# Kernel tuning notes

Hardware: AMD Instinct MI355X
Metric: run time of the kernel (lower is better)

## Reference

```python
import jax, jax.numpy as jnp
import numpy as np
from jax import lax

B, H, W = 8, 512, 512


def setup_inputs() -> dict:
    key = jax.random.key(0)
    k1, k2, k3, k4, k5 = jax.random.split(key, 5)
    img = jax.random.uniform(k1, (B, 3, H, W), jnp.float32)
    omega = 0.8 + 0.15 * jax.random.uniform(k2, (B, 1), jnp.float32)
    atmospheric_light = 0.5 + 0.5 * jax.random.uniform(k3, (B, 3), jnp.float32)
    L_low = 2.0 * jax.random.uniform(k4, (B, 1), jnp.float32)          # percent in [0,2)
    L_high = 95.0 + 4.0 * jax.random.uniform(k5, (B, 1), jnp.float32)  # percent in [95,99)
    guided_radius = 15  # python int, uniform across batch (original clamps to [1,50])
    return {"img": img, "omega": omega, "atmospheric_light": atmospheric_light,
            "L_low": L_low, "L_high": L_high, "guided_radius": guided_radius}


def _box_filter(x, r):
    # reflect-pad + mean over (2r+1)x(2r+1) window, separable (exactly avg_pool2d on reflect-padded input)
    k = 2 * r + 1
    xp = jnp.pad(x, ((0, 0), (0, 0), (r, r), (r, r)), mode='reflect')
    s = lax.reduce_window(xp, 0.0, lax.add, (1, 1, k, 1), (1, 1, 1, 1), 'VALID')
    s = lax.reduce_window(s, 0.0, lax.add, (1, 1, 1, k), (1, 1, 1, 1), 'VALID')
    return s / (k * k)


def _forward(img, omega, atmospheric_light, L_low, L_high, r):
    eps = 0.5
    Bb, Cc, Hh, Ww = img.shape
    A = atmospheric_light.reshape(Bb, 3, 1, 1)
    # initial transmission: t = 1 - omega * min_c(I/A)
    dark = jnp.min(img / (A + 1e-8), axis=1, keepdims=True)           # (B,1,H,W)
    t0 = 1.0 - omega.reshape(Bb, 1, 1, 1) * dark
    # gradient constraint (weights from t0, applied to shifted copies)
    wx = jnp.exp(-jnp.abs(t0[:, :, :, 1:] - t0[:, :, :, :-1]))
    tx = jnp.concatenate([t0[:, :, :, :1], t0[:, :, :, :-1] * wx], axis=3)
    wy = jnp.exp(-jnp.abs(t0[:, :, 1:, :] - t0[:, :, :-1, :]))
    tg = jnp.concatenate([tx[:, :, :1, :], tx[:, :, :-1, :] * wy], axis=2)
    # guided filter with grayscale guide
    rgb_w = jnp.array([0.299, 0.587, 0.114], dtype=img.dtype).reshape(1, 3, 1, 1)
    gray = jnp.sum(img * rgb_w, axis=1, keepdims=True)                # (B,1,H,W)
    mI = _box_filter(gray, r)
    mp = _box_filter(tg, r)
    mIp = _box_filter(gray * tg, r)
    cov_Ip = mIp - mI * mp
    var_I = _box_filter(gray * gray, r) - mI * mI
    a = cov_Ip / (var_I + eps)
    b = mp - a * mI
    t_final = jnp.clip(_box_filter(a, r) * gray + _box_filter(b, r), 0.1, 1.0)
    # restoration
    J = jnp.clip((img - A) / (t_final + 1e-8) + A, 0.0, 1.0)
    # percentile color stretch (vectorized over B and C)
    n = Hh * Ww
    svals = jnp.sort(J.reshape(Bb, Cc, n), axis=-1)
    li = jnp.clip((L_low / 100.0 * n).astype(jnp.int32), 0, n - 1)    # (B,1)
    hi = jnp.clip((L_high / 100.0 * n).astype(jnp.int32), 0, n - 1)
    p_low = jnp.take_along_axis(svals, jnp.broadcast_to(li[:, :, None], (Bb, Cc, 1)), axis=-1).reshape(Bb, Cc, 1, 1)
    p_high = jnp.take_along_axis(svals, jnp.broadcast_to(hi[:, :, None], (Bb, Cc, 1)), axis=-1).reshape(Bb, Cc, 1, 1)
    out = (jnp.clip(J, p_low, p_high) - p_low) / (p_high - p_low + 1e-8)
    return jnp.clip(out, 0.0, 1.0)


def reference(img, omega, atmospheric_light, L_low, L_high, guided_radius):
    r = max(1, min(int(guided_radius), 50))
    return _forward(img, omega, atmospheric_light, L_low, L_high, r)
```

## Files before the change

### kernel.cpp

```cpp
#include <hip/hip_runtime.h>
#include <cstdint>

constexpr int Bb = 8, Hh = 512, Ww = 512;
constexpr int HWn = Hh * Ww;
constexpr int CH1  = 8;
constexpr int CH23 = 16;
constexpr int CHK4 = 8;
constexpr int NBIN = 1024;

__device__ __forceinline__ int reflect_idx(int p, int n) {
    p = (p < 0) ? -p : p;
    return (p < n) ? p : (2 * n - 2 - p);
}
__device__ __forceinline__ int clamp_r(const int* rad) {
    int r = rad[0];
    return (r < 1) ? 1 : ((r > 50) ? 50 : r);
}

__global__ __launch_bounds__(512) void k1_stats_h(
    const float* __restrict__ img, const float* __restrict__ omega,
    const float* __restrict__ atm, const int* __restrict__ rad,
    float4* __restrict__ hq, unsigned int* __restrict__ histzero)
{
    const int tile = blockIdx.x;
    const int b = blockIdx.y;
    const int y0 = tile * CH1;
    const int j = threadIdx.x;
    const int fbid = b * gridDim.x + tile;
    if (fbid < 48) histzero[fbid * 512 + j] = 0u;
    const int r = clamp_r(rad);

    __shared__ float t0buf[2][512];
    __shared__ float4 Pb[512];
    __shared__ float4 wsum[8];

    const float om = omega[b];
    const float iA0 = 1.0f / (atm[b*3+0] + 1e-8f);
    const float iA1 = 1.0f / (atm[b*3+1] + 1e-8f);
    const float iA2 = 1.0f / (atm[b*3+2] + 1e-8f);
    const float* imb = img + (size_t)b * 3 * HWn;

    {
        const int yp = (y0 > 0) ? (y0 - 1) : 0;
        float r1 = imb[0*HWn + yp*Ww + j];
        float g1 = imb[1*HWn + yp*Ww + j];
        float b1 = imb[2*HWn + yp*Ww + j];
        t0buf[0][j] = 1.0f - om * fminf(fminf(r1*iA0, g1*iA1), b1*iA2);
    }
    __syncthreads();

    const int lane = j & 63, wv = j >> 6;
    int pv = 0;
    for (int k = 0; k < CH1; ++k) {
        const int y = y0 + k;
        float r0 = imb[0*HWn + y*Ww + j];
        float g0 = imb[1*HWn + y*Ww + j];
        float b0 = imb[2*HWn + y*Ww + j];
        float t0c = 1.0f - om * fminf(fminf(r0*iA0, g0*iA1), b0*iA2);
        float gr = 0.299f*r0 + 0.587f*g0 + 0.114f*b0;
        const float* t0p = t0buf[pv];
        t0buf[pv^1][j] = t0c;
        float tpj = t0p[j];
        float tx  = (j == 0) ? t0p[0] : t0p[j-1] * __expf(-fabsf(tpj - t0p[j-1]));
        float tgv = (y == 0) ? tx : tx * __expf(-fabsf(t0c - tpj));

        float4 incl;
        incl.x = gr; incl.y = tgv; incl.z = gr * tgv; incl.w = gr * gr;
        #pragma unroll
        for (int off = 1; off < 64; off <<= 1) {
            float ux = __shfl_up(incl.x, off);
            float uy = __shfl_up(incl.y, off);
            float uz = __shfl_up(incl.z, off);
            float uw = __shfl_up(incl.w, off);
            if (lane >= off) { incl.x += ux; incl.y += uy; incl.z += uz; incl.w += uw; }
        }
        if (lane == 63) wsum[wv] = incl;
        __syncthreads();
        float4 o4; o4.x = 0.f; o4.y = 0.f; o4.z = 0.f; o4.w = 0.f;
        #pragma unroll
        for (int w = 0; w < 7; ++w) {
            if (w < wv) {
                float4 t = wsum[w];
                o4.x += t.x; o4.y += t.y; o4.z += t.z; o4.w += t.w;
            }
        }
        float4 P; P.x = incl.x + o4.x; P.y = incl.y + o4.y; P.z = incl.z + o4.z; P.w = incl.w + o4.w;
        Pb[j] = P;
        __syncthreads();

        const int lo = j - r, hi = j + r;
        float4 s = Pb[(hi > 511) ? 511 : hi];
        if (lo > 0) {
            float4 t = Pb[lo-1];
            s.x -= t.x; s.y -= t.y; s.z -= t.z; s.w -= t.w;
        }
        if (lo < 0) {
            float4 t = Pb[r - j], u = Pb[0];
            s.x += t.x - u.x; s.y += t.y - u.y; s.z += t.z - u.z; s.w += t.w - u.w;
        }
        if (hi > 511) {
            float4 t = Pb[510], u = Pb[1021 - j - r];
            s.x += t.x - u.x; s.y += t.y - u.y; s.z += t.z - u.z; s.w += t.w - u.w;
        }
        hq[((size_t)b * Hh + y) * Ww + j] = s;
        pv ^= 1;
    }
}

__global__ __launch_bounds__(512) void k23_ab_h(
    const float4* __restrict__ hq, const int* __restrict__ rad,
    float2* __restrict__ hab)
{
    const int b  = blockIdx.y;
    const int y0 = blockIdx.x * CH23;
    const int j  = threadIdx.x;
    const int r  = clamp_r(rad);
    const float ikk = 1.0f / (float)((2*r+1) * (2*r+1));
    const int lane = j & 63, wv = j >> 6;

    __shared__ float2 Pb8[CH23][512];
    __shared__ float2 wsum8[CH23][8];

    const float4* hqb = hq + (size_t)b * Hh * Ww + j;
    float4 s; s.x = 0.f; s.y = 0.f; s.z = 0.f; s.w = 0.f;
    if (r == 15) {
        #pragma unroll
        for (int d = -15; d <= 15; ++d) {
            int m = reflect_idx(y0 + d, Hh);
            float4 v = hqb[(size_t)m * Ww];
            s.x += v.x; s.y += v.y; s.z += v.z; s.w += v.w;
        }
    } else {
        for (int d = -r; d <= r; ++d) {
            int m = reflect_idx(y0 + d, Hh);
            float4 v = hqb[(size_t)m * Ww];
            s.x += v.x; s.y += v.y; s.z += v.z; s.w += v.w;
        }
    }
    float av[CH23], bv[CH23];
    #pragma unroll
    for (int k = 0; k < CH23; ++k) {
        int y = y0 + k;
        float mI = s.x * ikk, mp = s.y * ikk, mIp = s.z * ikk, mII = s.w * ikk;
        float a = (mIp - mI * mp) / (mII - mI * mI + 0.5f);
        av[k] = a;
        bv[k] = mp - a * mI;
        int yin  = reflect_idx(y + 1 + r, Hh);
        int yout = reflect_idx(y - r, Hh);
        float4 vi = hqb[(size_t)yin  * Ww];
        float4 vo = hqb[(size_t)yout * Ww];
        s.x += vi.x - vo.x; s.y += vi.y - vo.y; s.z += vi.z - vo.z; s.w += vi.w - vo.w;
    }

    float ix[CH23], iy[CH23];
    #pragma unroll
    for (int k = 0; k < CH23; ++k) {
        float sx = av[k], sy = bv[k];
        #pragma unroll
        for (int off = 1; off < 64; off <<= 1) {
            float ux = __shfl_up(sx, off);
            float uy = __shfl_up(sy, off);
            if (lane >= off) { sx += ux; sy += uy; }
        }
        ix[k] = sx; iy[k] = sy;
        if (lane == 63) { wsum8[k][wv].x = sx; wsum8[k][wv].y = sy; }
    }
    __syncthreads();

    #pragma unroll
    for (int k = 0; k < CH23; ++k) {
        float ox = 0.f, oy = 0.f;
        #pragma unroll
        for (int w = 0; w < 7; ++w) {
            if (w < wv) { float2 t = wsum8[k][w]; ox += t.x; oy += t.y; }
        }
        Pb8[k][j].x = ix[k] + ox;
        Pb8[k][j].y = iy[k] + oy;
    }
    __syncthreads();

    const int lo = j - r, hi = j + r;
    const int him = (hi > 511) ? 511 : hi;
    #pragma unroll
    for (int k = 0; k < CH23; ++k) {
        float2 hs = Pb8[k][him];
        if (lo > 0)   { float2 t = Pb8[k][lo-1];  hs.x -= t.x; hs.y -= t.y; }
        if (lo < 0)   { float2 t = Pb8[k][r-j], u = Pb8[k][0];
                        hs.x += t.x - u.x; hs.y += t.y - u.y; }
        if (hi > 511) { float2 t = Pb8[k][510], u = Pb8[k][1021-j-r];
                        hs.x += t.x - u.x; hs.y += t.y - u.y; }
        hab[((size_t)b * Hh + (y0 + k)) * Ww + j] = hs;
    }
}

__global__ __launch_bounds__(256) void k4_final_v(
    const float4* __restrict__ hab4, const float2* __restrict__ img2,
    const float* __restrict__ atm, const int* __restrict__ rad,
    float2* __restrict__ J2, unsigned int* __restrict__ hist)
{
    const int b   = blockIdx.y;
    const int y0  = blockIdx.x * CHK4;
    const int tid = threadIdx.x;
    const int r   = clamp_r(rad);
    const float ikk = 1.0f / (float)((2*r+1) * (2*r+1));
    const int HP4 = Ww / 2;
    const int CP2 = HWn / 2;
    const int RP2 = Ww / 2;

    __shared__ unsigned int lh[3 * NBIN];
    for (int i = tid; i < 3 * NBIN; i += 256) lh[i] = 0u;
    __syncthreads();

    const float A0 = atm[b*3+0], A1 = atm[b*3+1], A2 = atm[b*3+2];
    const float2* imb = img2 + (size_t)b * 3 * CP2;
    float2*       Jb  = J2   + (size_t)b * 3 * CP2;
    const float4* habb = hab4 + (size_t)b * Hh * HP4 + tid;

    float2 V0, V1;
    V0.x = 0.f; V0.y = 0.f; V1.x = 0.f; V1.y = 0.f;
    if (r == 15) {
        #pragma unroll
        for (int d = -15; d <= 15; ++d) {
            int m = reflect_idx(y0 + d, Hh);
            float4 h = habb[(size_t)m * HP4];
            V0.x += h.x; V0.y += h.y; V1.x += h.z; V1.y += h.w;
        }
    } else {
        for (int d = -r; d <= r; ++d) {
            int m = reflect_idx(y0 + d, Hh);
            float4 h = habb[(size_t)m * HP4];
            V0.x += h.x; V0.y += h.y; V1.x += h.z; V1.y += h.w;
        }
    }

    unsigned int clo0 = 0, chi0 = 0, clo1 = 0, chi1 = 0, clo2 = 0, chi2 = 0;

    #pragma unroll
    for (int k = 0; k < CHK4; ++k) {
        const int y = y0 + k;
        const int yin  = reflect_idx(y + 1 + r, Hh);
        const int yout = reflect_idx(y - r, Hh);
        float4 hi4 = habb[(size_t)yin  * HP4];
        float4 ho4 = habb[(size_t)yout * HP4];
        const size_t po = (size_t)y * RP2 + tid;
        float2 c0 = imb[0*CP2 + po];
        float2 c1 = imb[1*CP2 + po];
        float2 c2 = imb[2*CP2 + po];

        float jr[2], jg[2], jb[2];
        {
            float g_ = 0.299f*c0.x + 0.587f*c1.x + 0.114f*c2.x;
            float t  = fminf(fmaxf((V0.x * g_ + V0.y) * ikk, 0.1f), 1.0f);
            float it = 1.0f / (t + 1e-8f);
            jr[0] = fminf(fmaxf((c0.x - A0) * it + A0, 0.f), 1.f);
            jg[0] = fminf(fmaxf((c1.x - A1) * it + A1, 0.f), 1.f);
            jb[0] = fminf(fmaxf((c2.x - A2) * it + A2, 0.f), 1.f);
        }
        {
            float g_ = 0.299f*c0.y + 0.587f*c1.y + 0.114f*c2.y;
            float t  = fminf(fmaxf((V1.x * g_ + V1.y) * ikk, 0.1f), 1.0f);
            float it = 1.0f / (t + 1e-8f);
            jr[1] = fminf(fmaxf((c0.y - A0) * it + A0, 0.f), 1.f);
            jg[1] = fminf(fmaxf((c1.y - A1) * it + A1, 0.f), 1.f);
            jb[1] = fminf(fmaxf((c2.y - A2) * it + A2, 0.f), 1.f);
        }
        Jb[0*CP2 + po] = make_float2(jr[0], jr[1]);
        Jb[1*CP2 + po] = make_float2(jg[0], jg[1]);
        Jb[2*CP2 + po] = make_float2(jb[0], jb[1]);

        #pragma unroll
        for (int q = 0; q < 2; ++q) {
            int bR = (int)(jr[q] * (float)NBIN); bR = (bR > NBIN-1) ? NBIN-1 : bR;
            if (bR == 0) clo0++; else if (bR == NBIN-1) chi0++; else atomicAdd(&lh[0*NBIN + bR], 1u);
            int bG = (int)(jg[q] * (float)NBIN); bG = (bG > NBIN-1) ? NBIN-1 : bG;
            if (bG == 0) clo1++; else if (bG == NBIN-1) chi1++; else atomicAdd(&lh[1*NBIN + bG], 1u);
            int bB = (int)(jb[q] * (float)NBIN); bB = (bB > NBIN-1) ? NBIN-1 : bB;
            if (bB == 0) clo2++; else if (bB == NBIN-1) chi2++; else atomicAdd(&lh[2*NBIN + bB], 1u);
        }

        V0.x += hi4.x - ho4.x; V0.y += hi4.y - ho4.y;
        V1.x += hi4.z - ho4.z; V1.y += hi4.w - ho4.w;
    }

    if (clo0) atomicAdd(&lh[0*NBIN],            clo0);
    if (chi0) atomicAdd(&lh[0*NBIN + NBIN - 1], chi0);
    if (clo1) atomicAdd(&lh[1*NBIN],            clo1);
    if (chi1) atomicAdd(&lh[1*NBIN + NBIN - 1], chi1);
    if (clo2) atomicAdd(&lh[2*NBIN],            clo2);
    if (chi2) atomicAdd(&lh[2*NBIN + NBIN - 1], chi2);
    __syncthreads();

    const size_t hb = (size_t)b * 3 * NBIN;
    for (int i = tid; i < 3 * NBIN; i += 256) {
        unsigned int v = lh[i];
        if (v) atomicAdd(&hist[hb + i], v);
    }
}

__global__ __launch_bounds__(256) void k6_norm(
    float4* __restrict__ J4, const unsigned int* __restrict__ hist,
    const float* __restrict__ L_low, const float* __restrict__ L_high)
{
    const int bc  = blockIdx.x >> 6;
    const int sub = blockIdx.x & 63;
    const int b   = bc / 3;
    __shared__ float sp[2];

    if (threadIdx.x < 64) {
        const int lane = threadIdx.x;
        const unsigned int* hb = hist + (size_t)bc * NBIN;
        unsigned int loc[NBIN / 64];
        unsigned int lsum = 0;
        #pragma unroll
        for (int i = 0; i < NBIN / 64; ++i) { loc[i] = hb[lane * (NBIN/64) + i]; lsum += loc[i]; }
        unsigned int incl = lsum;
        #pragma unroll
        for (int off = 1; off < 64; off <<= 1) {
            unsigned int v = __shfl_up(incl, off);
            if (lane >= off) incl += v;
        }
        unsigned int excl = incl - lsum;
        #pragma unroll
        for (int t = 0; t < 2; ++t) {
            float L = t ? L_high[b] : L_low[b];
            int k = (int)(L * (1.0f / 100.0f) * (float)HWn);
            k = (k < 0) ? 0 : ((k > HWn - 1) ? HWn - 1 : k);
            if ((unsigned int)k >= excl && (unsigned int)k < incl) {
                unsigned int c = excl;
                #pragma unroll
                for (int i = 0; i < NBIN / 64; ++i) {
                    if ((unsigned int)k < c + loc[i]) {
                        sp[t] = ((float)(lane * (NBIN/64) + i) + 0.5f) * (1.0f / (float)NBIN);
                        break;
                    }
                    c += loc[i];
                }
            }
        }
    }
    __syncthreads();

    const float l = sp[0], h = sp[1];
    const float inv = 1.0f / (h - l + 1e-8f);
    float4* base = J4 + (size_t)bc * (HWn / 4) + (size_t)sub * 1024;
    #pragma unroll
    for (int s = 0; s < 4; ++s) {
        const int idx = threadIdx.x + s * 256;
        float4 v = base[idx];
        v.x = fminf(fmaxf((fminf(fmaxf(v.x, l), h) - l) * inv, 0.f), 1.f);
        v.y = fminf(fmaxf((fminf(fmaxf(v.y, l), h) - l) * inv, 0.f), 1.f);
        v.z = fminf(fmaxf((fminf(fmaxf(v.z, l), h) - l) * inv, 0.f), 1.f);
        v.w = fminf(fmaxf((fminf(fmaxf(v.w, l), h) - l) * inv, 0.f), 1.f);
        base[idx] = v;
    }
}

extern "C" void kernel_launch(void* const* d_in, const int* in_sizes, int n_in,
                              void* d_out, int out_size, void* d_ws, size_t ws_size,
                              hipStream_t stream)
{
    const float* img    = (const float*)d_in[0];
    const float* omega  = (const float*)d_in[1];
    const float* atm    = (const float*)d_in[2];
    const float* L_low  = (const float*)d_in[3];
    const float* L_high = (const float*)d_in[4];
    const int*   rad    = (const int*)d_in[5];
    float* J  = (float*)d_out;
    float* ws = (float*)d_ws;

    const size_t F = (size_t)Bb * HWn;
    float4* hq  = (float4*)ws;
    float2* hab = (float2*)(ws + 4 * F);
    unsigned int* hist = (unsigned int*)(ws + 6 * F);

    k1_stats_h<<<dim3(Hh/CH1,  Bb), 512, 0, stream>>>(img, omega, atm, rad, hq, hist);
    k23_ab_h  <<<dim3(Hh/CH23, Bb), 512, 0, stream>>>(hq, rad, hab);
    k4_final_v<<<dim3(Hh/CHK4, Bb), 256, 0, stream>>>((const float4*)hab, (const float2*)img, atm, rad, (float2*)J, hist);
    k6_norm   <<<24 * 64, 256, 0, stream>>>((float4*)J, hist, L_low, L_high);
}
```

Baseline: 171.3 us.

## Replace vertical sliding-window sums with chunked prefix sums plus per-chunk totals

```diff
diff --git a/kernel.cpp b/kernel.cpp
--- a/kernel.cpp
+++ b/kernel.cpp
@@ -4,9 +4,10 @@
 constexpr int Bb = 8, Hh = 512, Ww = 512;
 constexpr int HWn = Hh * Ww;
 constexpr int CH1  = 8;
-constexpr int CH23 = 16;
-constexpr int CHK4 = 8;
+constexpr int CH23 = 8;
+constexpr int CHK4 = 4;
 constexpr int NBIN = 1024;
+constexpr int NCHK = Hh / 8;
 
 __device__ __forceinline__ int reflect_idx(int p, int n) {
     p = (p < 0) ? -p : p;
@@ -16,11 +17,47 @@
     int r = rad[0];
     return (r < 1) ? 1 : ((r > 50) ? 50 : r);
 }
+__device__ __forceinline__ float4 f4add(float4 a, float4 b) {
+    return make_float4(a.x + b.x, a.y + b.y, a.z + b.z, a.w + b.w);
+}
+__device__ __forceinline__ float4 f4sub(float4 a, float4 b) {
+    return make_float4(a.x - b.x, a.y - b.y, a.z - b.z, a.w - b.w);
+}
+
+__device__ __forceinline__ float4 ps_range(const float4* __restrict__ P,
+                                           const float4* __restrict__ T,
+                                           int a, int b, int pitch) {
+    float4 res = P[(size_t)b * pitch];
+    int cs;
+    if (a > 0) {
+        res = f4sub(res, P[(size_t)(a - 1) * pitch]);
+        cs = (a - 1) >> 3;
+    } else {
+        cs = 0;
+    }
+    const int cb = b >> 3;
+    for (int c = cs; c < cb; ++c)
+        res = f4add(res, T[(size_t)c * pitch]);
+    return res;
+}
+
+__device__ __forceinline__ float4 win_sum(const float4* __restrict__ P,
+                                          const float4* __restrict__ T,
+                                          int y, int r, int pitch) {
+    const int lo = y - r, hi = y + r;
+    const int a = lo < 0 ? 0 : lo;
+    const int b = hi > Hh - 1 ? Hh - 1 : hi;
+    float4 s = ps_range(P, T, a, b, pitch);
+    if (lo < 0)      s = f4add(s, ps_range(P, T, 1, -lo, pitch));
+    if (hi > Hh - 1) s = f4add(s, ps_range(P, T, 2 * Hh - 2 - hi, Hh - 2, pitch));
+    return s;
+}
 
 __global__ __launch_bounds__(512) void k1_stats_h(
     const float* __restrict__ img, const float* __restrict__ omega,
     const float* __restrict__ atm, const int* __restrict__ rad,
-    float4* __restrict__ hq, unsigned int* __restrict__ histzero)
+    float4* __restrict__ P1, float4* __restrict__ T1,
+    unsigned int* __restrict__ histzero)
 {
     const int tile = blockIdx.x;
     const int b = blockIdx.y;
@@ -51,6 +88,7 @@
 
     const int lane = j & 63, wv = j >> 6;
     int pv = 0;
+    float4 pacc = make_float4(0.f, 0.f, 0.f, 0.f);
     for (int k = 0; k < CH1; ++k) {
         const int y = y0 + k;
         float r0 = imb[0*HWn + y*Ww + j];
@@ -76,40 +114,32 @@
         }
         if (lane == 63) wsum[wv] = incl;
         __syncthreads();
-        float4 o4; o4.x = 0.f; o4.y = 0.f; o4.z = 0.f; o4.w = 0.f;
+        float4 o4 = make_float4(0.f, 0.f, 0.f, 0.f);
         #pragma unroll
         for (int w = 0; w < 7; ++w) {
-            if (w < wv) {
-                float4 t = wsum[w];
-                o4.x += t.x; o4.y += t.y; o4.z += t.z; o4.w += t.w;
-            }
-        }
-        float4 P; P.x = incl.x + o4.x; P.y = incl.y + o4.y; P.z = incl.z + o4.z; P.w = incl.w + o4.w;
+            if (w < wv) o4 = f4add(o4, wsum[w]);
+        }
+        float4 P = f4add(incl, o4);
         Pb[j] = P;
         __syncthreads();
 
         const int lo = j - r, hi = j + r;
         float4 s = Pb[(hi > 511) ? 511 : hi];
-        if (lo > 0) {
-            float4 t = Pb[lo-1];
-            s.x -= t.x; s.y -= t.y; s.z -= t.z; s.w -= t.w;
-        }
-        if (lo < 0) {
-            float4 t = Pb[r - j], u = Pb[0];
-            s.x += t.x - u.x; s.y += t.y - u.y; s.z += t.z - u.z; s.w += t.w - u.w;
-        }
-        if (hi > 511) {
-            float4 t = Pb[510], u = Pb[1021 - j - r];
-            s.x += t.x - u.x; s.y += t.y - u.y; s.z += t.z - u.z; s.w += t.w - u.w;
-        }
-        hq[((size_t)b * Hh + y) * Ww + j] = s;
+        if (lo > 0)   s = f4sub(s, Pb[lo-1]);
+        if (lo < 0)   s = f4add(s, f4sub(Pb[r - j], Pb[0]));
+        if (hi > 511) s = f4add(s, f4sub(Pb[510], Pb[1021 - j - r]));
+
+        pacc = f4add(pacc, s);
+        P1[((size_t)b * Hh + y) * Ww + j] = pacc;
         pv ^= 1;
     }
+    T1[((size_t)b * NCHK + tile) * Ww + j] = pacc;
 }
 
 __global__ __launch_bounds__(512) void k23_ab_h(
-    const float4* __restrict__ hq, const int* __restrict__ rad,
-    float2* __restrict__ hab)
+    const float4* __restrict__ P1, const float4* __restrict__ T1,
+    const int* __restrict__ rad,
+    float2* __restrict__ P2, float2* __restrict__ T2)
 {
     const int b  = blockIdx.y;
     const int y0 = blockIdx.x * CH23;
@@ -121,35 +151,36 @@
     __shared__ float2 Pb8[CH23][512];
     __shared__ float2 wsum8[CH23][8];
 
-    const float4* hqb = hq + (size_t)b * Hh * Ww + j;
-    float4 s; s.x = 0.f; s.y = 0.f; s.z = 0.f; s.w = 0.f;
-    if (r == 15) {
-        #pragma unroll
-        for (int d = -15; d <= 15; ++d) {
-            int m = reflect_idx(y0 + d, Hh);
-            float4 v = hqb[(size_t)m * Ww];
-            s.x += v.x; s.y += v.y; s.z += v.z; s.w += v.w;
+    const float4* Pj = P1 + (size_t)b * Hh * Ww + j;
+    const float4* Tj = T1 + (size_t)b * NCHK * Ww + j;
+
+    float av[CH23], bv[CH23];
+    if (r == 15 && y0 >= 16 && y0 <= Hh - 24) {
+        const int c0 = y0 >> 3;
+        float4 Ta = Tj[(size_t)(c0-2) * Ww];
+        float4 Tb = Tj[(size_t)(c0-1) * Ww];
+        float4 Tc = Tj[(size_t)(c0  ) * Ww];
+        float4 Td = Tj[(size_t)(c0+1) * Ww];
+        float4 TTb0 = f4add(f4add(Ta, Tb), Tc);
+        float4 TTb1 = f4add(TTb0, Td);
+        #pragma unroll
+        for (int k = 0; k < CH23; ++k) {
+            float4 Phi = Pj[(size_t)(y0 + k + 15) * Ww];
+            float4 Plo = Pj[(size_t)(y0 + k - 16) * Ww];
+            float4 W = f4sub(f4add(Phi, (k == 0) ? TTb0 : TTb1), Plo);
+            float mI = W.x * ikk, mp = W.y * ikk, mIp = W.z * ikk, mII = W.w * ikk;
+            float a = (mIp - mI * mp) / (mII - mI * mI + 0.5f);
+            av[k] = a;
+            bv[k] = mp - a * mI;
         }
     } else {
-        for (int d = -r; d <= r; ++d) {
-            int m = reflect_idx(y0 + d, Hh);
-            float4 v = hqb[(size_t)m * Ww];
-            s.x += v.x; s.y += v.y; s.z += v.z; s.w += v.w;
-        }
-    }
-    float av[CH23], bv[CH23];
-    #pragma unroll
-    for (int k = 0; k < CH23; ++k) {
-        int y = y0 + k;
-        float mI = s.x * ikk, mp = s.y * ikk, mIp = s.z * ikk, mII = s.w * ikk;
-        float a = (mIp - mI * mp) / (mII - mI * mI + 0.5f);
-        av[k] = a;
-        bv[k] = mp - a * mI;
-        int yin  = reflect_idx(y + 1 + r, Hh);
-        int yout = reflect_idx(y - r, Hh);
-        float4 vi = hqb[(size_t)yin  * Ww];
-        float4 vo = hqb[(size_t)yout * Ww];
-        s.x += vi.x - vo.x; s.y += vi.y - vo.y; s.z += vi.z - vo.z; s.w += vi.w - vo.w;
+        for (int k = 0; k < CH23; ++k) {
+            float4 W = win_sum(Pj, Tj, y0 + k, r, Ww);
+            float mI = W.x * ikk, mp = W.y * ikk, mIp = W.z * ikk, mII = W.w * ikk;
+            float a = (mIp - mI * mp) / (mII - mI * mI + 0.5f);
+            av[k] = a;
+            bv[k] = mp - a * mI;
+        }
     }
 
     float ix[CH23], iy[CH23];
@@ -181,6 +212,7 @@
 
     const int lo = j - r, hi = j + r;
     const int him = (hi > 511) ? 511 : hi;
+    float2 hacc; hacc.x = 0.f; hacc.y = 0.f;
     #pragma unroll
     for (int k = 0; k < CH23; ++k) {
         float2 hs = Pb8[k][him];
@@ -189,12 +221,15 @@
                         hs.x += t.x - u.x; hs.y += t.y - u.y; }
         if (hi > 511) { float2 t = Pb8[k][510], u = Pb8[k][1021-j-r];
                         hs.x += t.x - u.x; hs.y += t.y - u.y; }
-        hab[((size_t)b * Hh + (y0 + k)) * Ww + j] = hs;
-    }
+        hacc.x += hs.x; hacc.y += hs.y;
+        P2[((size_t)b * Hh + (y0 + k)) * Ww + j] = hacc;
+    }
+    T2[((size_t)b * NCHK + (y0 >> 3)) * Ww + j] = hacc;
 }
 
 __global__ __launch_bounds__(256) void k4_final_v(
-    const float4* __restrict__ hab4, const float2* __restrict__ img2,
+    const float4* __restrict__ P2f4, const float4* __restrict__ T2f4,
+    const float2* __restrict__ img2,
     const float* __restrict__ atm, const int* __restrict__ rad,
     float2* __restrict__ J2, unsigned int* __restrict__ hist)
 {
@@ -214,23 +249,29 @@
     const float A0 = atm[b*3+0], A1 = atm[b*3+1], A2 = atm[b*3+2];
     const float2* imb = img2 + (size_t)b * 3 * CP2;
     float2*       Jb  = J2   + (size_t)b * 3 * CP2;
-    const float4* habb = hab4 + (size_t)b * Hh * HP4 + tid;
-
-    float2 V0, V1;
-    V0.x = 0.f; V0.y = 0.f; V1.x = 0.f; V1.y = 0.f;
-    if (r == 15) {
-        #pragma unroll
-        for (int d = -15; d <= 15; ++d) {
-            int m = reflect_idx(y0 + d, Hh);
-            float4 h = habb[(size_t)m * HP4];
-            V0.x += h.x; V0.y += h.y; V1.x += h.z; V1.y += h.w;
+    const float4* Pj  = P2f4 + (size_t)b * Hh * HP4 + tid;
+    const float4* Tj  = T2f4 + (size_t)b * NCHK * HP4 + tid;
+
+    float4 Wk[CHK4];
+    if (r == 15 && y0 >= 16 && y0 <= Hh - 20) {
+        const int c0 = y0 >> 3;
+        const int off = y0 & 7;
+        float4 Ta = Tj[(size_t)(c0-2) * HP4];
+        float4 Tb = Tj[(size_t)(c0-1) * HP4];
+        float4 Tc = Tj[(size_t)(c0  ) * HP4];
+        float4 Td = Tj[(size_t)(c0+1) * HP4];
+        float4 TTb0 = f4add(f4add(Ta, Tb), Tc);
+        float4 TTb1 = f4add(TTb0, Td);
+        #pragma unroll
+        for (int k = 0; k < CHK4; ++k) {
+            float4 Phi = Pj[(size_t)(y0 + k + 15) * HP4];
+            float4 Plo = Pj[(size_t)(y0 + k - 16) * HP4];
+            Wk[k] = f4sub(f4add(Phi, (k == 0 && off == 0) ? TTb0 : TTb1), Plo);
         }
     } else {
-        for (int d = -r; d <= r; ++d) {
-            int m = reflect_idx(y0 + d, Hh);
-            float4 h = habb[(size_t)m * HP4];
-            V0.x += h.x; V0.y += h.y; V1.x += h.z; V1.y += h.w;
-        }
+        #pragma unroll
+        for (int k = 0; k < CHK4; ++k)
+            Wk[k] = win_sum(Pj, Tj, y0 + k, r, HP4);
     }
 
     unsigned int clo0 = 0, chi0 = 0, clo1 = 0, chi1 = 0, clo2 = 0, chi2 = 0;
@@ -238,31 +279,27 @@
     #pragma unroll
     for (int k = 0; k < CHK4; ++k) {
         const int y = y0 + k;
-        const int yin  = reflect_idx(y + 1 + r, Hh);
-        const int yout = reflect_idx(y - r, Hh);
-        float4 hi4 = habb[(size_t)yin  * HP4];
-        float4 ho4 = habb[(size_t)yout * HP4];
         const size_t po = (size_t)y * RP2 + tid;
-        float2 c0 = imb[0*CP2 + po];
-        float2 c1 = imb[1*CP2 + po];
-        float2 c2 = imb[2*CP2 + po];
+        float2 c0v = imb[0*CP2 + po];
+        float2 c1v = imb[1*CP2 + po];
+        float2 c2v = imb[2*CP2 + po];
 
         float jr[2], jg[2], jb[2];
         {
-            float g_ = 0.299f*c0.x + 0.587f*c1.x + 0.114f*c2.x;
-            float t  = fminf(fmaxf((V0.x * g_ + V0.y) * ikk, 0.1f), 1.0f);
+            float g_ = 0.299f*c0v.x + 0.587f*c1v.x + 0.114f*c2v.x;
+            float t  = fminf(fmaxf((Wk[k].x * g_ + Wk[k].y) * ikk, 0.1f), 1.0f);
             float it = 1.0f / (t + 1e-8f);
-            jr[0] = fminf(fmaxf((c0.x - A0) * it + A0, 0.f), 1.f);
-            jg[0] = fminf(fmaxf((c1.x - A1) * it + A1, 0.f), 1.f);
-            jb[0] = fminf(fmaxf((c2.x - A2) * it + A2, 0.f), 1.f);
+            jr[0] = fminf(fmaxf((c0v.x - A0) * it + A0, 0.f), 1.f);
+            jg[0] = fminf(fmaxf((c1v.x - A1) * it + A1, 0.f), 1.f);
+            jb[0] = fminf(fmaxf((c2v.x - A2) * it + A2, 0.f), 1.f);
         }
         {
-            float g_ = 0.299f*c0.y + 0.587f*c1.y + 0.114f*c2.y;
-            float t  = fminf(fmaxf((V1.x * g_ + V1.y) * ikk, 0.1f), 1.0f);
+            float g_ = 0.299f*c0v.y + 0.587f*c1v.y + 0.114f*c2v.y;
+            float t  = fminf(fmaxf((Wk[k].z * g_ + Wk[k].w) * ikk, 0.1f), 1.0f);
             float it = 1.0f / (t + 1e-8f);
-            jr[1] = fminf(fmaxf((c0.y - A0) * it + A0, 0.f), 1.f);
-            jg[1] = fminf(fmaxf((c1.y - A1) * it + A1, 0.f), 1.f);
-            jb[1] = fminf(fmaxf((c2.y - A2) * it + A2, 0.f), 1.f);
+            jr[1] = fminf(fmaxf((c0v.y - A0) * it + A0, 0.f), 1.f);
+            jg[1] = fminf(fmaxf((c1v.y - A1) * it + A1, 0.f), 1.f);
+            jb[1] = fminf(fmaxf((c2v.y - A2) * it + A2, 0.f), 1.f);
         }
         Jb[0*CP2 + po] = make_float2(jr[0], jr[1]);
         Jb[1*CP2 + po] = make_float2(jg[0], jg[1]);
@@ -277,9 +314,6 @@
             int bB = (int)(jb[q] * (float)NBIN); bB = (bB > NBIN-1) ? NBIN-1 : bB;
             if (bB == 0) clo2++; else if (bB == NBIN-1) chi2++; else atomicAdd(&lh[2*NBIN + bB], 1u);
         }
-
-        V0.x += hi4.x - ho4.x; V0.y += hi4.y - ho4.y;
-        V1.x += hi4.z - ho4.z; V1.y += hi4.w - ho4.w;
     }
 
     if (clo0) atomicAdd(&lh[0*NBIN],            clo0);
@@ -369,12 +403,16 @@
     float* ws = (float*)d_ws;
 
     const size_t F = (size_t)Bb * HWn;
-    float4* hq  = (float4*)ws;
-    float2* hab = (float2*)(ws + 4 * F);
-    unsigned int* hist = (unsigned int*)(ws + 6 * F);
-
-    k1_stats_h<<<dim3(Hh/CH1,  Bb), 512, 0, stream>>>(img, omega, atm, rad, hq, hist);
-    k23_ab_h  <<<dim3(Hh/CH23, Bb), 512, 0, stream>>>(hq, rad, hab);
-    k4_final_v<<<dim3(Hh/CHK4, Bb), 256, 0, stream>>>((const float4*)hab, (const float2*)img, atm, rad, (float2*)J, hist);
+    float4* P1 = (float4*)ws;
+    float2* P2 = (float2*)(ws + 4 * F);
+    float4* T1 = (float4*)(ws + 6 * F);
+    float2* T2 = (float2*)(ws + 6 * F + F / 2);
+    unsigned int* hist = (unsigned int*)(ws + 6 * F + F / 2 + F / 4);
+
+    k1_stats_h<<<dim3(Hh/CH1,  Bb), 512, 0, stream>>>(img, omega, atm, rad, P1, T1, hist);
+    k23_ab_h  <<<dim3(Hh/CH23, Bb), 512, 0, stream>>>(P1, T1, rad, P2, T2);
+    k4_final_v<<<dim3(Hh/CHK4, Bb), 256, 0, stream>>>((const float4*)P2, (const float4*)T2,
+                                                      (const float2*)img, atm, rad,
+                                                      (float2*)J, hist);
     k6_norm   <<<24 * 64, 256, 0, stream>>>((float4*)J, hist, L_low, L_high);
 }
```

New measurement: 169.4 us. No clear change (-1.1%).
